# Optimization experiments

Measured on AMD Instinct MI355X. Metric: run time of the kernel, lower is better.

Reference implementation:

```python
import jax, jax.numpy as jnp
import numpy as np

_SQRT_2_OVER_PI = 0.7978845608028654  # sqrt(2/pi)
_EPS = 1e-12  # F.normalize default eps


def _gelu_tanh(x):
    return 0.5 * x * (1.0 + jnp.tanh(_SQRT_2_OVER_PI * (x + 0.044715 * x * x * x)))


def _l2_normalize(v):
    n = jnp.linalg.norm(v, axis=-1, keepdims=True)
    return v / jnp.maximum(n, _EPS)


def setup_inputs() -> dict:
    key = jax.random.key(0)
    k_x, k_p = jax.random.split(key)
    B, T, D, K = 4, 4096, 4096, 256
    x = jax.random.normal(k_x, (B, T, D), dtype=jnp.float32)
    emas = jax.random.normal(k_p, (K, D), dtype=jnp.float32)
    log_tau = jnp.asarray(np.log(2.0), dtype=jnp.float32)           # GELU2_TEMP
    log_blend = jnp.asarray(np.log(0.3 / 0.7), dtype=jnp.float32)   # GELU2_BLEND logit
    logit_decay = jnp.asarray(np.log(0.9 / 0.1), dtype=jnp.float32) # GELU2_EMA_DECAY logit
    return {"x": x, "emas": emas, "log_tau": log_tau,
            "log_blend": log_blend, "logit_decay": logit_decay}


def reference(x, emas, log_tau, log_blend, logit_decay):
    # Steady-state (_ready=True) forward of GELU2.
    tau = jnp.exp(log_tau)
    alpha = jax.nn.sigmoid(log_blend)
    d = jax.nn.sigmoid(logit_decay)

    x_norm = _l2_normalize(x)          # (B,T,D)
    p_norm = _l2_normalize(emas)       # (K,D)
    sim = jnp.einsum('btd,kd->btk', x_norm, p_norm)  # (B,T,K)
    max_sim = jnp.max(sim, axis=-1)    # (B,T)
    novelty = jnp.exp(-tau * max_sim)  # (B,T)
    scale = 1.0 - alpha * d + alpha * d * novelty[..., None]  # (B,T,1)
    out = _gelu_tanh(x * scale)

    # Competitive EMA prototype update (detached, stateful in torch).
    x_mean = jnp.mean(x.reshape(-1, x.shape[-1]), axis=0)        # (D,)
    x_mean_n = _l2_normalize(x_mean[None, :])                    # (1,D)
    k_star = jnp.argmax(jnp.sum(p_norm * x_mean_n, axis=-1))     # scalar
    d_val = jax.lax.stop_gradient(d)
    new_row = d_val * emas[k_star] + (1.0 - d_val) * jax.lax.stop_gradient(x_mean)
    new_emas = emas.at[k_star].set(new_row)

    return out, new_emas
```

## Files before the change

### kernel.cpp

```cpp
#include <hip/hip_runtime.h>
#include <hip/hip_bf16.h>

typedef __bf16 bf16x8 __attribute__((ext_vector_type(8)));
typedef float  f32x4  __attribute__((ext_vector_type(4)));

#define N_ROWS 16384
#define DDIM   4096
#define KPROT  256
#define BM     32
#define BK     64
#define OUT0_ELEMS 67108864

#define WS_PB    0
#define WS_INV   2097152
#define WS_CSUM  2098176
#define WS_CELL  2114560

__device__ __forceinline__ unsigned f2bf2(float lo, float hi) {
    unsigned a = __float_as_uint(lo), b = __float_as_uint(hi);
    a = (a + 0x7FFFu + ((a >> 16) & 1u)) >> 16;
    b = (b + 0x7FFFu + ((b >> 16) & 1u)) >> 16;
    return a | (b << 16);
}

__device__ __forceinline__ float gelu_tanh(float y) {
    float z = 0.7978845608028654f * (y + 0.044715f * y * y * y);
    float t = __expf(2.f * z);
    float th = 1.f - __fdividef(2.f, t + 1.f);
    return 0.5f * y * (1.f + th);
}

__device__ __forceinline__ float sigmoidf(float v) {
    return 1.f / (1.f + __expf(-v));
}

__global__ void __launch_bounds__(256) prep_kernel(const float* __restrict__ emas,
                                                   unsigned* __restrict__ pb,
                                                   float* __restrict__ inv_norm) {
    const int k = blockIdx.x, t = threadIdx.x;
    const int lane = t & 63, w = t >> 6;
    const f32x4* er = (const f32x4*)(emas + (size_t)k * DDIM);
    f32x4 v[4];
    float ss = 0.f;
#pragma unroll
    for (int j = 0; j < 4; ++j) {
        v[j] = er[j * 256 + t];
        ss += v[j][0] * v[j][0] + v[j][1] * v[j][1] + v[j][2] * v[j][2] + v[j][3] * v[j][3];
    }
#pragma unroll
    for (int m = 1; m < 64; m <<= 1) ss += __shfl_xor(ss, m);
    __shared__ float red[4];
    if (lane == 0) red[w] = ss;
    __syncthreads();
    float tot = red[0] + red[1] + red[2] + red[3];
    float inv = 1.f / fmaxf(sqrtf(tot), 1e-12f);
    if (t == 0) inv_norm[k] = inv;
#pragma unroll
    for (int j = 0; j < 4; ++j) {
        uint2 p2;
        p2.x = f2bf2(v[j][0] * inv, v[j][1] * inv);
        p2.y = f2bf2(v[j][2] * inv, v[j][3] * inv);
        *(uint2*)(pb + (size_t)k * 2048 + (size_t)(j * 256 + t) * 2) = p2;
    }
}

__global__ void __launch_bounds__(256, 2)
main_kernel(const float* __restrict__ x, const unsigned* __restrict__ pb,
            const float* __restrict__ log_tau, const float* __restrict__ log_blend,
            const float* __restrict__ logit_decay,
            float* __restrict__ outp, float* __restrict__ colsum) {
    __shared__ __align__(16) unsigned lds_a[8 * BM * 4];
    __shared__ __align__(16) unsigned lds_b[8 * KPROT * 4];
    __shared__ float lds_wmax[4][BM];
    __shared__ float lds_sumsq[BM];
    __shared__ float lds_scale[BM];

    const int t = threadIdx.x;
    const int lane = t & 63, w = t >> 6;
    const int q = lane >> 4, rr = lane & 15;
    const int arow = t >> 3, ac = t & 7;
    const size_t row0 = (size_t)blockIdx.x * BM;

    const f32x4 zero = {0.f, 0.f, 0.f, 0.f};
    f32x4 acc[2][4];
#pragma unroll
    for (int rt = 0; rt < 2; ++rt)
#pragma unroll
        for (int ct = 0; ct < 4; ++ct) acc[rt][ct] = zero;

    float ss = 0.f;
    const float* xrow = x + (row0 + (size_t)arow) * DDIM + ac * 4;
    const unsigned* pbbase = pb + (size_t)arow * 2048 + ac * 4;

    for (int it = 0; it < DDIM / BK; ++it) {
        const int k0 = it * BK;
        f32x4 va = __builtin_nontemporal_load((const f32x4*)(xrow + k0));
        f32x4 vb = __builtin_nontemporal_load((const f32x4*)(xrow + k0 + 32));
        ss += va[0] * va[0] + va[1] * va[1] + va[2] * va[2] + va[3] * va[3];
        ss += vb[0] * vb[0] + vb[1] * vb[1] + vb[2] * vb[2] + vb[3] * vb[3];
        uint2 pa, pbv;
        pa.x = f2bf2(va[0], va[1]);  pa.y = f2bf2(va[2], va[3]);
        pbv.x = f2bf2(vb[0], vb[1]); pbv.y = f2bf2(vb[2], vb[3]);
        const int kca = ac >> 1, kcb = kca + 4;
        *(uint2*)&lds_a[kca * 128 + ((arow ^ kca) * 4) + (ac & 1) * 2] = pa;
        *(uint2*)&lds_a[kcb * 128 + ((arow ^ kcb) * 4) + (ac & 1) * 2] = pbv;
#pragma unroll
        for (int i = 0; i < 8; ++i) {
            const int n = arow + i * 32;
            int4 g = *(const int4*)(pbbase + (size_t)i * 65536 + it * 32);
            *(int4*)&lds_b[ac * 1024 + ((n ^ ac) * 4)] = g;
        }
        __syncthreads();
#pragma unroll
        for (int ks8 = 0; ks8 < 8; ks8 += 4) {
            const int kcq = ks8 + q;
            bf16x8 af[2], bfr[4];
            af[0] = *(const bf16x8*)&lds_a[kcq * 128 + ((rr ^ kcq) * 4)];
            af[1] = *(const bf16x8*)&lds_a[kcq * 128 + (((16 + rr) ^ kcq) * 4)];
#pragma unroll
            for (int ct = 0; ct < 4; ++ct) {
                const int n = w * 64 + ct * 16 + rr;
                bfr[ct] = *(const bf16x8*)&lds_b[kcq * 1024 + ((n ^ kcq) * 4)];
            }
#pragma unroll
            for (int rt = 0; rt < 2; ++rt)
#pragma unroll
                for (int ct = 0; ct < 4; ++ct)
                    acc[rt][ct] = __builtin_amdgcn_mfma_f32_16x16x32_bf16(
                        af[rt], bfr[ct], acc[rt][ct], 0, 0, 0);
        }
        __syncthreads();
    }

    ss += __shfl_xor(ss, 1); ss += __shfl_xor(ss, 2); ss += __shfl_xor(ss, 4);
    if (ac == 0) lds_sumsq[arow] = ss;

#pragma unroll
    for (int rt = 0; rt < 2; ++rt)
#pragma unroll
        for (int i = 0; i < 4; ++i) {
            float m = fmaxf(fmaxf(acc[rt][0][i], acc[rt][1][i]),
                            fmaxf(acc[rt][2][i], acc[rt][3][i]));
            m = fmaxf(m, __shfl_xor(m, 1));
            m = fmaxf(m, __shfl_xor(m, 2));
            m = fmaxf(m, __shfl_xor(m, 4));
            m = fmaxf(m, __shfl_xor(m, 8));
            if (rr == 0) lds_wmax[w][rt * 16 + q * 4 + i] = m;
        }
    __syncthreads();

    if (t < BM) {
        float m = fmaxf(fmaxf(lds_wmax[0][t], lds_wmax[1][t]),
                        fmaxf(lds_wmax[2][t], lds_wmax[3][t]));
        float nrm = fmaxf(sqrtf(lds_sumsq[t]), 1e-12f);
        float msim = m / nrm;
        float tau = __expf(log_tau[0]);
        float ad = sigmoidf(log_blend[0]) * sigmoidf(logit_decay[0]);
        lds_scale[t] = 1.f - ad + ad * __expf(-tau * msim);
    }
    __syncthreads();

    float cs[4][4];
#pragma unroll
    for (int j = 0; j < 4; ++j)
#pragma unroll
        for (int e = 0; e < 4; ++e) cs[j][e] = 0.f;

    for (int r = 0; r < BM; ++r) {
        const float s = lds_scale[r];
        const f32x4* xr = (const f32x4*)(x + (row0 + (size_t)r) * DDIM);
        f32x4* orow = (f32x4*)(outp + (row0 + (size_t)r) * DDIM);
#pragma unroll
        for (int j = 0; j < 4; ++j) {
            f32x4 v = __builtin_nontemporal_load(&xr[j * 256 + t]);
            cs[j][0] += v[0]; cs[j][1] += v[1]; cs[j][2] += v[2]; cs[j][3] += v[3];
            f32x4 g;
            g[0] = gelu_tanh(v[0] * s); g[1] = gelu_tanh(v[1] * s);
            g[2] = gelu_tanh(v[2] * s); g[3] = gelu_tanh(v[3] * s);
            __builtin_nontemporal_store(g, &orow[j * 256 + t]);
        }
    }
#pragma unroll
    for (int j = 0; j < 4; ++j)
#pragma unroll
        for (int e = 0; e < 4; ++e)
            atomicAdd(&colsum[j * 1024 + t * 4 + e], cs[j][e]);
}

__global__ void __launch_bounds__(256) argmax_kernel(const float* __restrict__ emas,
                                                     const float* __restrict__ colsum,
                                                     const float* __restrict__ inv_norm,
                                                     unsigned long long* __restrict__ cell) {
    const int k = blockIdx.x, t = threadIdx.x;
    const int lane = t & 63, w = t >> 6;
    const f32x4* er = (const f32x4*)(emas + (size_t)k * DDIM);
    const f32x4* cr = (const f32x4*)colsum;
    float s = 0.f;
#pragma unroll
    for (int j = 0; j < 4; ++j) {
        f32x4 a = er[j * 256 + t], b = cr[j * 256 + t];
        s += a[0] * b[0] + a[1] * b[1] + a[2] * b[2] + a[3] * b[3];
    }
#pragma unroll
    for (int m = 1; m < 64; m <<= 1) s += __shfl_xor(s, m);
    __shared__ float red[4];
    if (lane == 0) red[w] = s;
    __syncthreads();
    if (t == 0) {
        float dotv = (red[0] + red[1] + red[2] + red[3]) * inv_norm[k];
        unsigned u = __float_as_uint(dotv);
        unsigned key = (u & 0x80000000u) ? ~u : (u | 0x80000000u);
        unsigned long long pk = ((unsigned long long)key << 32) |
                                (unsigned long long)(unsigned)(~k);
        atomicMax(cell, pk);
    }
}

__global__ void __launch_bounds__(256) final_kernel(const float* __restrict__ emas,
                                                    const float* __restrict__ colsum,
                                                    const unsigned long long* __restrict__ cell,
                                                    const float* __restrict__ logit_decay,
                                                    float* __restrict__ out2) {
    const int idx = blockIdx.x * 256 + threadIdx.x;
    const int e = idx * 4;
    const int k = e >> 12, d0 = e & 4095;
    f32x4 v = *(const f32x4*)(emas + e);
    const unsigned kstar = ~(unsigned)(*cell);
    if ((unsigned)k == kstar) {
        const float dd = sigmoidf(logit_decay[0]);
        const float od = (1.f - dd) * (1.f / 16384.f);
        f32x4 xm = *(const f32x4*)(colsum + d0);
        v[0] = dd * v[0] + od * xm[0];
        v[1] = dd * v[1] + od * xm[1];
        v[2] = dd * v[2] + od * xm[2];
        v[3] = dd * v[3] + od * xm[3];
    }
    *(f32x4*)(out2 + e) = v;
}

extern "C" void kernel_launch(void* const* d_in, const int* in_sizes, int n_in,
                              void* d_out, int out_size, void* d_ws, size_t ws_size,
                              hipStream_t stream) {
    const float* x           = (const float*)d_in[0];
    const float* emas        = (const float*)d_in[1];
    const float* log_tau     = (const float*)d_in[2];
    const float* log_blend   = (const float*)d_in[3];
    const float* logit_decay = (const float*)d_in[4];
    float* outp     = (float*)d_out;
    float* out_emas = outp + (size_t)OUT0_ELEMS;

    char* ws = (char*)d_ws;
    unsigned* pb                 = (unsigned*)(ws + WS_PB);
    float* inv_norm              = (float*)(ws + WS_INV);
    float* colsum                = (float*)(ws + WS_CSUM);
    unsigned long long* cell     = (unsigned long long*)(ws + WS_CELL);

    (void)hipMemsetAsync(colsum, 0, 16384 + 8, stream);

    prep_kernel<<<KPROT, 256, 0, stream>>>(emas, pb, inv_norm);
    main_kernel<<<N_ROWS / BM, 256, 0, stream>>>(x, pb, log_tau, log_blend,
                                                 logit_decay, outp, colsum);
    argmax_kernel<<<KPROT, 256, 0, stream>>>(emas, colsum, inv_norm, cell);
    final_kernel<<<KPROT * DDIM / 1024, 256, 0, stream>>>(emas, colsum, cell,
                                                          logit_decay, out_emas);
}
```

Before: 598.0 us.

## Double-buffer LDS tiles and stage prototypes with direct global-to-LDS loads

```diff
diff --git a/kernel.cpp b/kernel.cpp
--- a/kernel.cpp
+++ b/kernel.cpp
@@ -9,6 +9,7 @@
 #define KPROT  256
 #define BM     32
 #define BK     64
+#define NIT    (DDIM / BK)
 #define OUT0_ELEMS 67108864
 
 #define WS_PB    0
@@ -32,6 +33,12 @@
 
 __device__ __forceinline__ float sigmoidf(float v) {
     return 1.f / (1.f + __expf(-v));
+}
+
+__device__ __forceinline__ void glds16(const unsigned* src, unsigned* dst) {
+    __builtin_amdgcn_global_load_lds(
+        (const __attribute__((address_space(1))) void*)src,
+        (__attribute__((address_space(3))) void*)dst, 16, 0, 0);
 }
 
 __global__ void __launch_bounds__(256) prep_kernel(const float* __restrict__ emas,
@@ -64,13 +71,50 @@
     }
 }
 
+__device__ __forceinline__ void mfma_phase(const unsigned* __restrict__ la,
+                                           const unsigned* __restrict__ lb,
+                                           f32x4 (&acc)[2][4],
+                                           int q, int rr, int w) {
+#pragma unroll
+    for (int ks8 = 0; ks8 < 8; ks8 += 4) {
+        const int kcq = ks8 + q;
+        bf16x8 af[2], bfr[4];
+        af[0] = *(const bf16x8*)&la[kcq * 128 + ((rr ^ kcq) * 4)];
+        af[1] = *(const bf16x8*)&la[kcq * 128 + (((16 + rr) ^ kcq) * 4)];
+#pragma unroll
+        for (int ct = 0; ct < 4; ++ct) {
+            const int n = w * 64 + ct * 16 + rr;
+            bfr[ct] = *(const bf16x8*)&lb[kcq * 1024 + ((n ^ kcq) * 4)];
+        }
+#pragma unroll
+        for (int rt = 0; rt < 2; ++rt)
+#pragma unroll
+            for (int ct = 0; ct < 4; ++ct)
+                acc[rt][ct] = __builtin_amdgcn_mfma_f32_16x16x32_bf16(
+                    af[rt], bfr[ct], acc[rt][ct], 0, 0, 0);
+    }
+}
+
+__device__ __forceinline__ float finish_a(unsigned* __restrict__ la,
+                                          f32x4 va, f32x4 vb,
+                                          int arow, int kca, int kcb, int ah) {
+    float ss = va[0] * va[0] + va[1] * va[1] + va[2] * va[2] + va[3] * va[3]
+             + vb[0] * vb[0] + vb[1] * vb[1] + vb[2] * vb[2] + vb[3] * vb[3];
+    uint2 pa, pbv;
+    pa.x = f2bf2(va[0], va[1]);  pa.y = f2bf2(va[2], va[3]);
+    pbv.x = f2bf2(vb[0], vb[1]); pbv.y = f2bf2(vb[2], vb[3]);
+    *(uint2*)&la[kca * 128 + ((arow ^ kca) * 4) + ah] = pa;
+    *(uint2*)&la[kcb * 128 + ((arow ^ kcb) * 4) + ah] = pbv;
+    return ss;
+}
+
 __global__ void __launch_bounds__(256, 2)
 main_kernel(const float* __restrict__ x, const unsigned* __restrict__ pb,
             const float* __restrict__ log_tau, const float* __restrict__ log_blend,
             const float* __restrict__ logit_decay,
             float* __restrict__ outp, float* __restrict__ colsum) {
-    __shared__ __align__(16) unsigned lds_a[8 * BM * 4];
-    __shared__ __align__(16) unsigned lds_b[8 * KPROT * 4];
+    __shared__ __align__(16) unsigned lds_a[2][8 * BM * 4];
+    __shared__ __align__(16) unsigned lds_b[2][8 * KPROT * 4];
     __shared__ float lds_wmax[4][BM];
     __shared__ float lds_sumsq[BM];
     __shared__ float lds_scale[BM];
@@ -79,6 +123,7 @@
     const int lane = t & 63, w = t >> 6;
     const int q = lane >> 4, rr = lane & 15;
     const int arow = t >> 3, ac = t & 7;
+    const int kca = ac >> 1, kcb = kca + 4, ah = (ac & 1) * 2;
     const size_t row0 = (size_t)blockIdx.x * BM;
 
     const f32x4 zero = {0.f, 0.f, 0.f, 0.f};
@@ -88,49 +133,46 @@
 #pragma unroll
         for (int ct = 0; ct < 4; ++ct) acc[rt][ct] = zero;
 
-    float ss = 0.f;
     const float* xrow = x + (row0 + (size_t)arow) * DDIM + ac * 4;
-    const unsigned* pbbase = pb + (size_t)arow * 2048 + ac * 4;
-
-    for (int it = 0; it < DDIM / BK; ++it) {
-        const int k0 = it * BK;
+
+#define BOFF(i) (((((((i) & 3) * 64) + lane) ^ (2 * w + ((i) >> 2))) * 2048u) \
+                 + (unsigned)(2 * w + ((i) >> 2)) * 4u)
+    const unsigned bo0 = BOFF(0), bo1 = BOFF(1), bo2 = BOFF(2), bo3 = BOFF(3);
+    const unsigned bo4 = BOFF(4), bo5 = BOFF(5), bo6 = BOFF(6), bo7 = BOFF(7);
+#undef BOFF
+
+#define STAGE_B(buf, itk) do {                                            \
+        const unsigned ko = (unsigned)(itk) * 32u;                        \
+        glds16(pb + bo0 + ko, &lds_b[buf][(w * 8 + 0) * 256]);            \
+        glds16(pb + bo1 + ko, &lds_b[buf][(w * 8 + 1) * 256]);            \
+        glds16(pb + bo2 + ko, &lds_b[buf][(w * 8 + 2) * 256]);            \
+        glds16(pb + bo3 + ko, &lds_b[buf][(w * 8 + 3) * 256]);            \
+        glds16(pb + bo4 + ko, &lds_b[buf][(w * 8 + 4) * 256]);            \
+        glds16(pb + bo5 + ko, &lds_b[buf][(w * 8 + 5) * 256]);            \
+        glds16(pb + bo6 + ko, &lds_b[buf][(w * 8 + 6) * 256]);            \
+        glds16(pb + bo7 + ko, &lds_b[buf][(w * 8 + 7) * 256]);            \
+    } while (0)
+
+    float ss;
+    {
+        f32x4 va = __builtin_nontemporal_load((const f32x4*)(xrow));
+        f32x4 vb = __builtin_nontemporal_load((const f32x4*)(xrow + 32));
+        STAGE_B(0, 0);
+        ss = finish_a(lds_a[0], va, vb, arow, kca, kcb, ah);
+    }
+    __syncthreads();
+
+    for (int it = 0; it < NIT - 1; ++it) {
+        const int cur = it & 1, nxt = cur ^ 1;
+        const int k0 = (it + 1) * BK;
         f32x4 va = __builtin_nontemporal_load((const f32x4*)(xrow + k0));
         f32x4 vb = __builtin_nontemporal_load((const f32x4*)(xrow + k0 + 32));
-        ss += va[0] * va[0] + va[1] * va[1] + va[2] * va[2] + va[3] * va[3];
-        ss += vb[0] * vb[0] + vb[1] * vb[1] + vb[2] * vb[2] + vb[3] * vb[3];
-        uint2 pa, pbv;
-        pa.x = f2bf2(va[0], va[1]);  pa.y = f2bf2(va[2], va[3]);
-        pbv.x = f2bf2(vb[0], vb[1]); pbv.y = f2bf2(vb[2], vb[3]);
-        const int kca = ac >> 1, kcb = kca + 4;
-        *(uint2*)&lds_a[kca * 128 + ((arow ^ kca) * 4) + (ac & 1) * 2] = pa;
-        *(uint2*)&lds_a[kcb * 128 + ((arow ^ kcb) * 4) + (ac & 1) * 2] = pbv;
-#pragma unroll
-        for (int i = 0; i < 8; ++i) {
-            const int n = arow + i * 32;
-            int4 g = *(const int4*)(pbbase + (size_t)i * 65536 + it * 32);
-            *(int4*)&lds_b[ac * 1024 + ((n ^ ac) * 4)] = g;
-        }
+        STAGE_B(nxt, it + 1);
+        mfma_phase(lds_a[cur], lds_b[cur], acc, q, rr, w);
+        ss += finish_a(lds_a[nxt], va, vb, arow, kca, kcb, ah);
         __syncthreads();
-#pragma unroll
-        for (int ks8 = 0; ks8 < 8; ks8 += 4) {
-            const int kcq = ks8 + q;
-            bf16x8 af[2], bfr[4];
-            af[0] = *(const bf16x8*)&lds_a[kcq * 128 + ((rr ^ kcq) * 4)];
-            af[1] = *(const bf16x8*)&lds_a[kcq * 128 + (((16 + rr) ^ kcq) * 4)];
-#pragma unroll
-            for (int ct = 0; ct < 4; ++ct) {
-                const int n = w * 64 + ct * 16 + rr;
-                bfr[ct] = *(const bf16x8*)&lds_b[kcq * 1024 + ((n ^ kcq) * 4)];
-            }
-#pragma unroll
-            for (int rt = 0; rt < 2; ++rt)
-#pragma unroll
-                for (int ct = 0; ct < 4; ++ct)
-                    acc[rt][ct] = __builtin_amdgcn_mfma_f32_16x16x32_bf16(
-                        af[rt], bfr[ct], acc[rt][ct], 0, 0, 0);
-        }
-        __syncthreads();
-    }
+    }
+    mfma_phase(lds_a[1], lds_b[1], acc, q, rr, w);
 
     ss += __shfl_xor(ss, 1); ss += __shfl_xor(ss, 2); ss += __shfl_xor(ss, 4);
     if (ac == 0) lds_sumsq[arow] = ss;
```

New measurement: 654.3 us. 9.4% more time.
